# Kernel tuning notes

Measured on AMD Instinct MI355X. Metric: run time of the kernel, lower is better.

The kernel has to match this reference:

```python
import jax, jax.numpy as jnp
import numpy as np

TOTAL_WORDS = 10000
EMBED_LEN = 100
SEQ_LEN = 80
UNITS = 512
BATCH = 1024


def gru_layer(x_seq, Wx, Wh, b):
    """Keras GRU (reset_after=True), x_seq: [T, B, D] -> ys: [T, B, U]."""
    bi, br = b[0], b[1]  # input bias, recurrent bias, each [3U]
    U = Wh.shape[0]

    def step(h, x_t):
        gx = x_t @ Wx + bi            # [B, 3U]
        gh = h @ Wh + br              # [B, 3U]
        xz, xr, xh = gx[:, :U], gx[:, U:2 * U], gx[:, 2 * U:]
        hz, hr, hn = gh[:, :U], gh[:, U:2 * U], gh[:, 2 * U:]
        z = jax.nn.sigmoid(xz + hz)
        r = jax.nn.sigmoid(xr + hr)
        hh = jnp.tanh(xh + r * hn)
        h_new = z * h + (1.0 - z) * hh
        return h_new, h_new

    h0 = jnp.zeros((x_seq.shape[1], U), dtype=x_seq.dtype)
    _, ys = jax.lax.scan(step, h0, x_seq)
    return ys


def setup_inputs() -> dict:
    key = jax.random.key(0)
    ks = jax.random.split(key, 10)
    tokens = jax.random.randint(ks[0], (BATCH, SEQ_LEN), 0, TOTAL_WORDS, dtype=jnp.int32)
    s_e = 1.0 / np.sqrt(EMBED_LEN)
    s_u = 1.0 / np.sqrt(UNITS)
    emb = jax.random.normal(ks[1], (TOTAL_WORDS, EMBED_LEN), jnp.float32) * 0.05
    Wx1 = jax.random.normal(ks[2], (EMBED_LEN, 3 * UNITS), jnp.float32) * s_e
    Wh1 = jax.random.normal(ks[3], (UNITS, 3 * UNITS), jnp.float32) * s_u
    b1 = jnp.zeros((2, 3 * UNITS), jnp.float32)
    Wx2 = jax.random.normal(ks[4], (UNITS, 3 * UNITS), jnp.float32) * s_u
    Wh2 = jax.random.normal(ks[5], (UNITS, 3 * UNITS), jnp.float32) * s_u
    b2 = jnp.zeros((2, 3 * UNITS), jnp.float32)
    Wfc = jax.random.normal(ks[6], (UNITS, 1), jnp.float32) * s_u
    bfc = jnp.zeros((1,), jnp.float32)
    return {"tokens": tokens, "emb": emb, "Wx1": Wx1, "Wh1": Wh1, "b1": b1,
            "Wx2": Wx2, "Wh2": Wh2, "b2": b2, "Wfc": Wfc, "bfc": bfc}


def reference(tokens, emb, Wx1, Wh1, b1, Wx2, Wh2, b2, Wfc, bfc):
    x = emb[tokens]                       # [B, T, E]
    x = jnp.transpose(x, (1, 0, 2))       # [T, B, E] (scan over time)
    ys1 = gru_layer(x, Wx1, Wh1, b1)      # [T, B, U] return_sequences
    ys2 = gru_layer(ys1, Wx2, Wh2, b2)    # [T, B, U]
    h_last = ys2[-1]                      # [B, U] (last timestep only)
    logits = h_last @ Wfc + bfc           # [B, 1]
    return jax.nn.sigmoid(logits)
```

## Files before the change

### kernel.cpp

```cpp
#include <hip/hip_runtime.h>
#include <hip/hip_bf16.h>
#include <math.h>

typedef float f32x4 __attribute__((ext_vector_type(4)));
typedef int   ix4  __attribute__((ext_vector_type(4)));

#define MFMAI8(a,b,c) __builtin_amdgcn_mfma_i32_16x16x64_i8(a,b,c,0,0,0)

constexpr int BATCH = 1024, SEQ = 80, EMB = 100, U = 512;
constexpr int KC1 = 10;
constexpr int KC2 = 16;
constexpr float EMBMAX = 0.32f;
constexpr float INV127SQ = 1.f / 16129.f;

__device__ __forceinline__ float sigf_(float x) {
  return __builtin_amdgcn_rcpf(1.f + __expf(-x));
}
__device__ __forceinline__ float tanhf_(float x) {
  return fmaf(2.f, __builtin_amdgcn_rcpf(1.f + __expf(-2.f * x)), -1.f);
}

__global__ void k_colmax(const float* __restrict__ Wh1, const float* __restrict__ Wx1,
                         const float* __restrict__ Wh2, const float* __restrict__ Wx2,
                         float* __restrict__ scales) {
  int idx = blockIdx.x * 256 + threadIdx.x;
  if (idx >= 4 * 8 * 1536) return;
  int col = idx % 1536;
  int rest = idx / 1536;
  int kseg = rest & 7, m = rest >> 3;
  const float* W = (m == 0) ? Wh1 : (m == 1) ? Wx1 : (m == 2) ? Wh2 : Wx2;
  int Klim = (m == 1) ? EMB : 512;
  int k0 = kseg * 64, k1 = min(k0 + 64, Klim);
  float mx = 0.f;
  for (int k = k0; k < k1; ++k) mx = fmaxf(mx, fabsf(W[(size_t)k * 1536 + col]));
  if (k1 > k0) atomicMax((int*)&scales[m * 1536 + col], __float_as_int(mx));
}

__device__ __forceinline__ void pack_one(const float* __restrict__ WH,
                                         const float* __restrict__ WX,
                                         const float* __restrict__ scH,
                                         const float* __restrict__ scX,
                                         signed char* __restrict__ out,
                                         int KCH, int KCX, int KXr, int c) {
  int KC = KCH + KCX;
  int lane = c & 63;
  int rest = c >> 6;
  int g = rest % 3; rest /= 3;
  int kc = rest % KC;
  int u16 = rest / KC;
  int col = g * 512 + u16 * 16 + (lane & 15);
  int kl = (lane >> 4) * 16;
  float sH = 127.f / fmaxf(scH[col], 1e-12f);
  float sX = 127.f / fmaxf(scX[col], 1e-12f);
  ix4 v;
  signed char* vb = (signed char*)&v;
#pragma unroll
  for (int e = 0; e < 16; ++e) {
    int q = 0;
    if (kc < KCH) {
      int k = kc * 64 + kl + e;
      q = (int)rintf(WH[(size_t)k * 1536 + col] * sH);
    } else {
      int kx = (kc - KCH) * 64 + kl + e;
      if (kx < KXr) q = (int)rintf(WX[(size_t)kx * 1536 + col] * sX);
    }
    vb[e] = (signed char)q;
  }
  *(ix4*)(out + (size_t)c * 16) = v;
}

__global__ void k_prep(const float* __restrict__ Wh1, const float* __restrict__ Wx1,
                       const float* __restrict__ Wh2, const float* __restrict__ Wx2,
                       const float* __restrict__ scales,
                       signed char* __restrict__ wf1, signed char* __restrict__ wf2,
                       const float* __restrict__ emb, signed char* __restrict__ embq) {
  int b = blockIdx.x, tid = threadIdx.x;
  if (b < 240) {
    int c = b * 256 + tid;
    if (c < 61440) pack_one(Wh1, Wx1, scales, scales + 1536, wf1, 8, 2, EMB, c);
  } else if (b < 624) {
    int c = (b - 240) * 256 + tid;
    if (c < 98304) pack_one(Wh2, Wx2, scales + 3072, scales + 4608, wf2, 8, 8, U, c);
  } else {
    int idx = (b - 624) * 256 + tid;
    if (idx < 320000) {
      int r = idx >> 5, c4 = (idx & 31) * 4;
      char q[4];
#pragma unroll
      for (int j = 0; j < 4; ++j) {
        int c = c4 + j, v = 0;
        if (c < EMB) {
          float x = emb[r * EMB + c] * (127.f / EMBMAX);
          v = (int)rintf(fminf(127.f, fmaxf(-127.f, x)));
        }
        q[j] = (char)v;
      }
      *(int*)(embq + (size_t)r * 128 + c4) = *(int*)q;
    }
  }
}


__device__ __forceinline__ unsigned llc_read(const unsigned* p) {
  unsigned v;
  asm volatile("global_load_dword %0, %1, off sc0 sc1\n\ts_waitcnt vmcnt(0)"
               : "=v"(v) : "v"(p) : "memory");
  return v;
}

__device__ __forceinline__ void bar_arrive(unsigned* cnt, bool fast) {
  asm volatile("s_waitcnt vmcnt(0)" ::: "memory");
  __syncthreads();
  if (threadIdx.x == 0) {
    if (!fast) __builtin_amdgcn_fence(__ATOMIC_RELEASE, "agent");
    __hip_atomic_fetch_add(cnt, 1u, __ATOMIC_RELAXED, __HIP_MEMORY_SCOPE_AGENT);
  }
}

__device__ __forceinline__ void bar_wait(const unsigned* cnt, unsigned tgt, bool fast) {
  if (threadIdx.x == 0) {
    int spin = 0;
    while (llc_read(cnt) < tgt) {
      __builtin_amdgcn_s_sleep(1);
      if (++spin > (1 << 22)) break;
    }
    if (fast) {
      asm volatile("buffer_inv sc0\n\ts_waitcnt vmcnt(0)" ::: "memory");
    } else {
      __builtin_amdgcn_fence(__ATOMIC_ACQUIRE, "agent");
    }
  }
  __syncthreads();
}

__global__ __launch_bounds__(512, 2)
void k_gru_persist(const int* __restrict__ tokens, const signed char* __restrict__ embq,
                   const signed char* __restrict__ wf1, const signed char* __restrict__ wf2,
                   const float* __restrict__ b1, const float* __restrict__ b2,
                   const float* __restrict__ scales,
                   signed char* __restrict__ h1b0, signed char* __restrict__ h1b1,
                   signed char* __restrict__ h2b0, signed char* __restrict__ h2b1,
                   const float* __restrict__ Wfc, const float* __restrict__ bfc,
                   float* __restrict__ out, unsigned* __restrict__ bar) {
  __shared__ __attribute__((aligned(16))) signed char wt2[2 * KC2 * 3 * 1024];
  __shared__ unsigned char s_x[256];
  __shared__ int s_gl;

  const int bid = blockIdx.x, tid = threadIdx.x;

  {
    ix4* hz = (ix4*)(h1b0 + (size_t)bid * 8192);
    hz[tid] = (ix4){0, 0, 0, 0};
  }

  unsigned* xslot = bar + 1024;
  unsigned* gcnt  = bar + 1536;
  unsigned xcc = 0;
  asm volatile("s_getreg_b32 %0, hwreg(HW_REG_XCC_ID)" : "=s"(xcc));
  if (tid == 0)
    __hip_atomic_store(&xslot[bid], xcc + 1u, __ATOMIC_RELAXED, __HIP_MEMORY_SCOPE_AGENT);

  __syncthreads();
  if (tid == 0) {
    __builtin_amdgcn_fence(__ATOMIC_RELEASE, "agent");
    __hip_atomic_fetch_add(gcnt, 1u, __ATOMIC_RELAXED, __HIP_MEMORY_SCOPE_AGENT);
    int spin = 0;
    while (__hip_atomic_load(gcnt, __ATOMIC_RELAXED, __HIP_MEMORY_SCOPE_AGENT) < 256u) {
      __builtin_amdgcn_s_sleep(8);
      if (++spin > (1 << 24)) break;
    }
    __builtin_amdgcn_fence(__ATOMIC_ACQUIRE, "agent");
  }
  __syncthreads();

  if (tid < 256)
    s_x[tid] = (unsigned char)__hip_atomic_load(&xslot[tid], __ATOMIC_RELAXED,
                                                __HIP_MEMORY_SCOPE_AGENT);
  __syncthreads();
  if (tid == 0) {
    int cnts[8] = {0, 0, 0, 0, 0, 0, 0, 0};
    int r = 0;
    unsigned char mex = (unsigned char)(xcc + 1u);
    for (int b = 0; b < 256; ++b) {
      unsigned char v = s_x[b];
      if (v >= 1 && v <= 8) cnts[v - 1]++;
      if (b < bid && v == mex) r++;
    }
    int ok = 1;
    for (int j = 0; j < 8; ++j) ok &= (cnts[j] == 32);
    int gg, ll;
    if (ok) { gg = (int)xcc * 2 + (r >> 4); ll = r & 15; }
    else    { gg = bid & 15;                ll = bid >> 4; }
    s_gl = (gg << 9) | (ll << 1) | ok;
  }
  __syncthreads();
  const int g = s_gl >> 9, lb = (s_gl >> 1) & 15;
  const bool fastbar = (s_gl & 1) != 0;
  const int r0 = g * 64;
  unsigned* cnt1 = bar + g * 64;
  unsigned* cnt2 = bar + g * 64 + 32;

  {
    const ix4* s2 = (const ix4*)(wf2 + (size_t)lb * 6144 * 16);
    ix4* d2 = (ix4*)wt2;
    for (int i = tid; i < 6144; i += 512) d2[i] = s2[i];
  }

  const int wv = tid >> 6, lane = tid & 63, ln = lane & 15, quad = lane >> 4;
  const int rt = wv >> 1, uh = wv & 1;
  const int u16 = lb * 2 + uh;
  const int rw0 = r0 + rt * 16;
  const int kq = quad * 16;

  ix4 w1[30];
  {
    const ix4* s1 = (const ix4*)(wf1 + (size_t)u16 * KC1 * 3 * 1024);
#pragma unroll
    for (int f = 0; f < 30; ++f) w1[f] = s1[f * 64 + lane];
  }
  const signed char* wt2h = wt2 + uh * (KC2 * 3 * 1024) + lane * 16;

  const int u = u16 * 16 + ln;
  const float* sc_h1 = scales, *sc_x1 = scales + 1536, *sc_h2 = scales + 3072, *sc_x2 = scales + 4608;
  const float fz1h = sc_h1[u] * INV127SQ,        fz1x = sc_x1[u] * (EMBMAX * INV127SQ);
  const float fr1h = sc_h1[512 + u] * INV127SQ,  fr1x = sc_x1[512 + u] * (EMBMAX * INV127SQ);
  const float fn1h = sc_h1[1024 + u] * INV127SQ, fn1x = sc_x1[1024 + u] * (EMBMAX * INV127SQ);
  const float fz2h = sc_h2[u] * INV127SQ,        fz2x = sc_x2[u] * INV127SQ;
  const float fr2h = sc_h2[512 + u] * INV127SQ,  fr2x = sc_x2[512 + u] * INV127SQ;
  const float fn2h = sc_h2[1024 + u] * INV127SQ, fn2x = sc_x2[1024 + u] * INV127SQ;
  const float bz1 = b1[u] + b1[1536 + u],       br1 = b1[512 + u] + b1[2048 + u];
  const float bn1x = b1[1024 + u],              bn1h = b1[2560 + u];
  const float bz2 = b2[u] + b2[1536 + u],       br2 = b2[512 + u] + b2[2048 + u];
  const float bn2x = b2[1024 + u],              bn2h = b2[2560 + u];
  const size_t wb8 = (size_t)(u >> 6) * 65536 + (u & 63);

  float h1st[4] = {0.f, 0.f, 0.f, 0.f};
  float h2st[4] = {0.f, 0.f, 0.f, 0.f};

  ix4 z1x = (ix4){0,0,0,0}, r1x = (ix4){0,0,0,0}, n1x = (ix4){0,0,0,0};
  {
    int tok = tokens[(size_t)(rw0 + ln) * SEQ];
#pragma unroll
    for (int kc = 0; kc < 2; ++kc) {
      ix4 a = *(const ix4*)(embq + (size_t)tok * 128 + kc * 64 + kq);
      z1x = MFMAI8(a, w1[(8 + kc) * 3 + 0], z1x);
      r1x = MFMAI8(a, w1[(8 + kc) * 3 + 1], r1x);
      n1x = MFMAI8(a, w1[(8 + kc) * 3 + 2], n1x);
    }
  }

#pragma unroll 1
  for (int s = 0; s <= SEQ; ++s) {
    const signed char* h1r = (s & 1) ? h1b0 : h1b1;
    signed char*       h1w = (s & 1) ? h1b1 : h1b0;
    const signed char* h2r = (s & 1) ? h2b1 : h2b0;
    signed char*       h2w = (s & 1) ? h2b0 : h2b1;

    bar_wait(cnt1, 16u * (unsigned)s, fastbar);

    ix4 z1h = (ix4){0,0,0,0}, r1h = (ix4){0,0,0,0}, n1h = (ix4){0,0,0,0};
    ix4 z2x = (ix4){0,0,0,0}, r2x = (ix4){0,0,0,0}, n2x = (ix4){0,0,0,0};
#pragma unroll
    for (int kc = 0; kc < 8; ++kc) {
      ix4 a = *(const ix4*)(h1r + (size_t)kc * 65536 + (rw0 + ln) * 64 + kq);
      z1h = MFMAI8(a, w1[kc * 3 + 0], z1h);
      r1h = MFMAI8(a, w1[kc * 3 + 1], r1h);
      n1h = MFMAI8(a, w1[kc * 3 + 2], n1h);
      z2x = MFMAI8(a, *(const ix4*)(wt2h + ((8 + kc) * 3 + 0) * 1024), z2x);
      r2x = MFMAI8(a, *(const ix4*)(wt2h + ((8 + kc) * 3 + 1) * 1024), r2x);
      n2x = MFMAI8(a, *(const ix4*)(wt2h + ((8 + kc) * 3 + 2) * 1024), n2x);
    }
    if (s < SEQ) {
#pragma unroll
      for (int i = 0; i < 4; ++i) {
        int row = rw0 + quad * 4 + i;
        float z = sigf_(fmaf(fz1h, (float)z1h[i], fmaf(fz1x, (float)z1x[i], bz1)));
        float r = sigf_(fmaf(fr1h, (float)r1h[i], fmaf(fr1x, (float)r1x[i], br1)));
        float hh = tanhf_(fmaf(fn1x, (float)n1x[i], bn1x) +
                          r * fmaf(fn1h, (float)n1h[i], bn1h));
        float hn = hh + z * (h1st[i] - hh);
        h1st[i] = hn;
        h1w[wb8 + (size_t)row * 64] = (signed char)(int)rintf(hn * 127.f);
      }
    }
    bar_arrive(cnt1, fastbar);

    bar_wait(cnt2, 16u * (unsigned)s, fastbar);

    ix4 z2h = (ix4){0,0,0,0}, r2h = (ix4){0,0,0,0}, n2h = (ix4){0,0,0,0};
#pragma unroll
    for (int kc = 0; kc < 8; ++kc) {
      ix4 a = *(const ix4*)(h2r + (size_t)kc * 65536 + (rw0 + ln) * 64 + kq);
      z2h = MFMAI8(a, *(const ix4*)(wt2h + (kc * 3 + 0) * 1024), z2h);
      r2h = MFMAI8(a, *(const ix4*)(wt2h + (kc * 3 + 1) * 1024), r2h);
      n2h = MFMAI8(a, *(const ix4*)(wt2h + (kc * 3 + 2) * 1024), n2h);
    }
    if (s >= 1) {
#pragma unroll
      for (int i = 0; i < 4; ++i) {
        int row = rw0 + quad * 4 + i;
        float z = sigf_(fmaf(fz2h, (float)z2h[i], fmaf(fz2x, (float)z2x[i], bz2)));
        float r = sigf_(fmaf(fr2h, (float)r2h[i], fmaf(fr2x, (float)r2x[i], br2)));
        float hh = tanhf_(fmaf(fn2x, (float)n2x[i], bn2x) +
                          r * fmaf(fn2h, (float)n2h[i], bn2h));
        float hn = hh + z * (h2st[i] - hh);
        h2st[i] = hn;
        h2w[wb8 + (size_t)row * 64] = (signed char)(int)rintf(hn * 127.f);
      }
    }
    bar_arrive(cnt2, fastbar);

    if (s < SEQ - 1) {
      int tok = tokens[(size_t)(rw0 + ln) * SEQ + (s + 1)];
      z1x = (ix4){0,0,0,0}; r1x = (ix4){0,0,0,0}; n1x = (ix4){0,0,0,0};
#pragma unroll
      for (int kc = 0; kc < 2; ++kc) {
        ix4 a = *(const ix4*)(embq + (size_t)tok * 128 + kc * 64 + kq);
        z1x = MFMAI8(a, w1[(8 + kc) * 3 + 0], z1x);
        r1x = MFMAI8(a, w1[(8 + kc) * 3 + 1], r1x);
        n1x = MFMAI8(a, w1[(8 + kc) * 3 + 2], n1x);
      }
    }
  }

  bar_wait(cnt2, 16u * (unsigned)(SEQ + 1), fastbar);

  if (wv < 4) {
    int row = r0 + lb * 4 + wv;
    float sfc = 0.f;
#pragma unroll
    for (int j = 0; j < 8; ++j) {
      int k = j * 64 + lane;
      sfc += (float)h2b1[(size_t)j * 65536 + row * 64 + lane] * Wfc[k];
    }
#pragma unroll
    for (int off = 32; off; off >>= 1) sfc += __shfl_down(sfc, off, 64);
    if (lane == 0) out[row] = sigf_(sfc * (1.f / 127.f) + bfc[0]);
  }
}

extern "C" void kernel_launch(void* const* d_in, const int* in_sizes, int n_in,
                              void* d_out, int out_size, void* d_ws, size_t ws_size,
                              hipStream_t stream) {
  const int*   tokens = (const int*)d_in[0];
  const float* emb = (const float*)d_in[1];
  const float* Wx1 = (const float*)d_in[2];
  const float* Wh1 = (const float*)d_in[3];
  const float* b1  = (const float*)d_in[4];
  const float* Wx2 = (const float*)d_in[5];
  const float* Wh2 = (const float*)d_in[6];
  const float* b2  = (const float*)d_in[7];
  const float* Wfc = (const float*)d_in[8];
  const float* bfc = (const float*)d_in[9];
  float* out = (float*)d_out;

  signed char* wf1  = (signed char*)d_ws;
  signed char* wf2  = wf1 + 983040;
  signed char* embq = wf2 + 1572864;
  float* scales     = (float*)(embq + 1280000);
  unsigned* bar     = (unsigned*)((signed char*)scales + 24576);
  signed char* h1b0 = (signed char*)bar + 8192;
  signed char* h1b1 = h1b0 + 524288;
  signed char* h2b0 = h1b1 + 524288;
  signed char* h2b1 = h2b0 + 524288;

  hipMemsetAsync(scales, 0, 24576 + 8192, stream);

  k_colmax<<<(4 * 8 * 1536 + 255) / 256, 256, 0, stream>>>(Wh1, Wx1, Wh2, Wx2, scales);
  k_prep<<<1874, 256, 0, stream>>>(Wh1, Wx1, Wh2, Wx2, scales, wf1, wf2, emb, embq);

  void* args[] = {(void*)&tokens, (void*)&embq, (void*)&wf1, (void*)&wf2,
                  (void*)&b1, (void*)&b2, (void*)&scales,
                  (void*)&h1b0, (void*)&h1b1, (void*)&h2b0, (void*)&h2b1,
                  (void*)&Wfc, (void*)&bfc, (void*)&out, (void*)&bar};
  hipLaunchCooperativeKernel((void*)k_gru_persist, dim3(256), dim3(512), args, 0, stream);
}
```

Measured before the change: 587.2 us.

## Merge two per-step group barriers into one and unroll timestep pairs

Each timestep previously used two barriers: layer 1 finished and published h1 before layer 2 read h2. Now both h1 and h2 fragments are loaded right after a single barrier wait, all MFMAs for both layers are issued, and one arrive ends the step. This is possible because layer 2 at step s reads only h2 from step s-1. The loop is also unrolled in pairs through a macro so the ping-pong buffer pointers are fixed at compile time, and the XCC-aware group remapping is replaced by a fixed bid&15 grouping with a same-XCC check that decides whether the fast barrier is used. The cost is more live registers for the preloaded A fragments, and possibly fewer groups qualifying for the fast barrier path.

```diff
diff --git a/kernel.cpp b/kernel.cpp
--- a/kernel.cpp
+++ b/kernel.cpp
@@ -147,6 +147,9 @@
   __shared__ int s_gl;
 
   const int bid = blockIdx.x, tid = threadIdx.x;
+  const int g = bid & 15, lb = bid >> 4;
+  const int r0 = g * 64;
+  unsigned* cnt = bar + g * 64;
 
   {
     ix4* hz = (ix4*)(h1b0 + (size_t)bid * 8192);
@@ -178,27 +181,13 @@
                                                 __HIP_MEMORY_SCOPE_AGENT);
   __syncthreads();
   if (tid == 0) {
-    int cnts[8] = {0, 0, 0, 0, 0, 0, 0, 0};
-    int r = 0;
-    unsigned char mex = (unsigned char)(xcc + 1u);
-    for (int b = 0; b < 256; ++b) {
-      unsigned char v = s_x[b];
-      if (v >= 1 && v <= 8) cnts[v - 1]++;
-      if (b < bid && v == mex) r++;
-    }
-    int ok = 1;
-    for (int j = 0; j < 8; ++j) ok &= (cnts[j] == 32);
-    int gg, ll;
-    if (ok) { gg = (int)xcc * 2 + (r >> 4); ll = r & 15; }
-    else    { gg = bid & 15;                ll = bid >> 4; }
-    s_gl = (gg << 9) | (ll << 1) | ok;
-  }
-  __syncthreads();
-  const int g = s_gl >> 9, lb = (s_gl >> 1) & 15;
-  const bool fastbar = (s_gl & 1) != 0;
-  const int r0 = g * 64;
-  unsigned* cnt1 = bar + g * 64;
-  unsigned* cnt2 = bar + g * 64 + 32;
+    unsigned char x0 = s_x[g];
+    int f = (x0 != 0);
+    for (int j = 1; j < 16; ++j) f &= (s_x[g + 16 * j] == x0);
+    s_gl = f;
+  }
+  __syncthreads();
+  const bool fastbar = (s_gl != 0);
 
   {
     const ix4* s2 = (const ix4*)(wf2 + (size_t)lb * 6144 * 16);
@@ -211,6 +200,7 @@
   const int u16 = lb * 2 + uh;
   const int rw0 = r0 + rt * 16;
   const int kq = quad * 16;
+  const int aoff = (rw0 + ln) * 64 + kq;
 
   ix4 w1[30];
   {
@@ -249,81 +239,83 @@
     }
   }
 
+#define GRU_STEP(S, H1R, H1W, H2R, H2W)                                        \
+  {                                                                            \
+    bar_wait(cnt, 16u * (unsigned)(S), fastbar);                               \
+    ix4 a1[8], a2[8];                                                          \
+    _Pragma("unroll")                                                          \
+    for (int kc = 0; kc < 8; ++kc)                                             \
+      a1[kc] = *(const ix4*)((H1R) + (size_t)kc * 65536 + aoff);               \
+    _Pragma("unroll")                                                          \
+    for (int kc = 0; kc < 8; ++kc)                                             \
+      a2[kc] = *(const ix4*)((H2R) + (size_t)kc * 65536 + aoff);               \
+    ix4 z1h = (ix4){0,0,0,0}, r1h = (ix4){0,0,0,0}, n1h = (ix4){0,0,0,0};      \
+    ix4 z2x = (ix4){0,0,0,0}, r2x = (ix4){0,0,0,0}, n2x = (ix4){0,0,0,0};      \
+    ix4 z2h = (ix4){0,0,0,0}, r2h = (ix4){0,0,0,0}, n2h = (ix4){0,0,0,0};      \
+    _Pragma("unroll")                                                          \
+    for (int kc = 0; kc < 8; ++kc) {                                           \
+      z1h = MFMAI8(a1[kc], w1[kc * 3 + 0], z1h);                               \
+      r1h = MFMAI8(a1[kc], w1[kc * 3 + 1], r1h);                               \
+      n1h = MFMAI8(a1[kc], w1[kc * 3 + 2], n1h);                               \
+      z2x = MFMAI8(a1[kc], *(const ix4*)(wt2h + ((8 + kc) * 3 + 0) * 1024), z2x); \
+      r2x = MFMAI8(a1[kc], *(const ix4*)(wt2h + ((8 + kc) * 3 + 1) * 1024), r2x); \
+      n2x = MFMAI8(a1[kc], *(const ix4*)(wt2h + ((8 + kc) * 3 + 2) * 1024), n2x); \
+    }                                                                          \
+    _Pragma("unroll")                                                          \
+    for (int kc = 0; kc < 8; ++kc) {                                           \
+      z2h = MFMAI8(a2[kc], *(const ix4*)(wt2h + (kc * 3 + 0) * 1024), z2h);    \
+      r2h = MFMAI8(a2[kc], *(const ix4*)(wt2h + (kc * 3 + 1) * 1024), r2h);    \
+      n2h = MFMAI8(a2[kc], *(const ix4*)(wt2h + (kc * 3 + 2) * 1024), n2h);    \
+    }                                                                          \
+    if ((S) < SEQ) {                                                           \
+      _Pragma("unroll")                                                        \
+      for (int i = 0; i < 4; ++i) {                                            \
+        int row = rw0 + quad * 4 + i;                                          \
+        float z = sigf_(fmaf(fz1h, (float)z1h[i], fmaf(fz1x, (float)z1x[i], bz1))); \
+        float r = sigf_(fmaf(fr1h, (float)r1h[i], fmaf(fr1x, (float)r1x[i], br1))); \
+        float hh = tanhf_(fmaf(fn1x, (float)n1x[i], bn1x) +                    \
+                          r * fmaf(fn1h, (float)n1h[i], bn1h));                \
+        float hn = hh + z * (h1st[i] - hh);                                    \
+        h1st[i] = hn;                                                          \
+        (H1W)[wb8 + (size_t)row * 64] = (signed char)(int)rintf(hn * 127.f);   \
+      }                                                                        \
+    }                                                                          \
+    if ((S) >= 1) {                                                            \
+      _Pragma("unroll")                                                        \
+      for (int i = 0; i < 4; ++i) {                                            \
+        int row = rw0 + quad * 4 + i;                                          \
+        float z = sigf_(fmaf(fz2h, (float)z2h[i], fmaf(fz2x, (float)z2x[i], bz2))); \
+        float r = sigf_(fmaf(fr2h, (float)r2h[i], fmaf(fr2x, (float)r2x[i], br2))); \
+        float hh = tanhf_(fmaf(fn2x, (float)n2x[i], bn2x) +                    \
+                          r * fmaf(fn2h, (float)n2h[i], bn2h));                \
+        float hn = hh + z * (h2st[i] - hh);                                    \
+        h2st[i] = hn;                                                          \
+        (H2W)[wb8 + (size_t)row * 64] = (signed char)(int)rintf(hn * 127.f);   \
+      }                                                                        \
+    }                                                                          \
+    bar_arrive(cnt, fastbar);                                                  \
+    if ((S) < SEQ - 1) {                                                       \
+      int tok = tokens[(size_t)(rw0 + ln) * SEQ + ((S) + 1)];                  \
+      z1x = (ix4){0,0,0,0}; r1x = (ix4){0,0,0,0}; n1x = (ix4){0,0,0,0};        \
+      _Pragma("unroll")                                                        \
+      for (int kc = 0; kc < 2; ++kc) {                                         \
+        ix4 a = *(const ix4*)(embq + (size_t)tok * 128 + kc * 64 + kq);        \
+        z1x = MFMAI8(a, w1[(8 + kc) * 3 + 0], z1x);                            \
+        r1x = MFMAI8(a, w1[(8 + kc) * 3 + 1], r1x);                            \
+        n1x = MFMAI8(a, w1[(8 + kc) * 3 + 2], n1x);                            \
+      }                                                                        \
+    }                                                                          \
+  }
+
 #pragma unroll 1
-  for (int s = 0; s <= SEQ; ++s) {
-    const signed char* h1r = (s & 1) ? h1b0 : h1b1;
-    signed char*       h1w = (s & 1) ? h1b1 : h1b0;
-    const signed char* h2r = (s & 1) ? h2b1 : h2b0;
-    signed char*       h2w = (s & 1) ? h2b0 : h2b1;
-
-    bar_wait(cnt1, 16u * (unsigned)s, fastbar);
-
-    ix4 z1h = (ix4){0,0,0,0}, r1h = (ix4){0,0,0,0}, n1h = (ix4){0,0,0,0};
-    ix4 z2x = (ix4){0,0,0,0}, r2x = (ix4){0,0,0,0}, n2x = (ix4){0,0,0,0};
-#pragma unroll
-    for (int kc = 0; kc < 8; ++kc) {
-      ix4 a = *(const ix4*)(h1r + (size_t)kc * 65536 + (rw0 + ln) * 64 + kq);
-      z1h = MFMAI8(a, w1[kc * 3 + 0], z1h);
-      r1h = MFMAI8(a, w1[kc * 3 + 1], r1h);
-      n1h = MFMAI8(a, w1[kc * 3 + 2], n1h);
-      z2x = MFMAI8(a, *(const ix4*)(wt2h + ((8 + kc) * 3 + 0) * 1024), z2x);
-      r2x = MFMAI8(a, *(const ix4*)(wt2h + ((8 + kc) * 3 + 1) * 1024), r2x);
-      n2x = MFMAI8(a, *(const ix4*)(wt2h + ((8 + kc) * 3 + 2) * 1024), n2x);
-    }
-    if (s < SEQ) {
-#pragma unroll
-      for (int i = 0; i < 4; ++i) {
-        int row = rw0 + quad * 4 + i;
-        float z = sigf_(fmaf(fz1h, (float)z1h[i], fmaf(fz1x, (float)z1x[i], bz1)));
-        float r = sigf_(fmaf(fr1h, (float)r1h[i], fmaf(fr1x, (float)r1x[i], br1)));
-        float hh = tanhf_(fmaf(fn1x, (float)n1x[i], bn1x) +
-                          r * fmaf(fn1h, (float)n1h[i], bn1h));
-        float hn = hh + z * (h1st[i] - hh);
-        h1st[i] = hn;
-        h1w[wb8 + (size_t)row * 64] = (signed char)(int)rintf(hn * 127.f);
-      }
-    }
-    bar_arrive(cnt1, fastbar);
-
-    bar_wait(cnt2, 16u * (unsigned)s, fastbar);
-
-    ix4 z2h = (ix4){0,0,0,0}, r2h = (ix4){0,0,0,0}, n2h = (ix4){0,0,0,0};
-#pragma unroll
-    for (int kc = 0; kc < 8; ++kc) {
-      ix4 a = *(const ix4*)(h2r + (size_t)kc * 65536 + (rw0 + ln) * 64 + kq);
-      z2h = MFMAI8(a, *(const ix4*)(wt2h + (kc * 3 + 0) * 1024), z2h);
-      r2h = MFMAI8(a, *(const ix4*)(wt2h + (kc * 3 + 1) * 1024), r2h);
-      n2h = MFMAI8(a, *(const ix4*)(wt2h + (kc * 3 + 2) * 1024), n2h);
-    }
-    if (s >= 1) {
-#pragma unroll
-      for (int i = 0; i < 4; ++i) {
-        int row = rw0 + quad * 4 + i;
-        float z = sigf_(fmaf(fz2h, (float)z2h[i], fmaf(fz2x, (float)z2x[i], bz2)));
-        float r = sigf_(fmaf(fr2h, (float)r2h[i], fmaf(fr2x, (float)r2x[i], br2)));
-        float hh = tanhf_(fmaf(fn2x, (float)n2x[i], bn2x) +
-                          r * fmaf(fn2h, (float)n2h[i], bn2h));
-        float hn = hh + z * (h2st[i] - hh);
-        h2st[i] = hn;
-        h2w[wb8 + (size_t)row * 64] = (signed char)(int)rintf(hn * 127.f);
-      }
-    }
-    bar_arrive(cnt2, fastbar);
-
-    if (s < SEQ - 1) {
-      int tok = tokens[(size_t)(rw0 + ln) * SEQ + (s + 1)];
-      z1x = (ix4){0,0,0,0}; r1x = (ix4){0,0,0,0}; n1x = (ix4){0,0,0,0};
-#pragma unroll
-      for (int kc = 0; kc < 2; ++kc) {
-        ix4 a = *(const ix4*)(embq + (size_t)tok * 128 + kc * 64 + kq);
-        z1x = MFMAI8(a, w1[(8 + kc) * 3 + 0], z1x);
-        r1x = MFMAI8(a, w1[(8 + kc) * 3 + 1], r1x);
-        n1x = MFMAI8(a, w1[(8 + kc) * 3 + 2], n1x);
-      }
-    }
-  }
-
-  bar_wait(cnt2, 16u * (unsigned)(SEQ + 1), fastbar);
+  for (int sb = 0; sb < SEQ; sb += 2) {
+    GRU_STEP(sb,     h1b1, h1b0, h2b0, h2b1);
+    GRU_STEP(sb + 1, h1b0, h1b1, h2b1, h2b0);
+  }
+  GRU_STEP(SEQ, h1b1, h1b0, h2b0, h2b1);
+#undef GRU_STEP
+
+  bar_wait(cnt, 16u * (unsigned)(SEQ + 1), fastbar);
 
   if (wv < 4) {
     int row = r0 + lb * 4 + wv;
```

Result: slower. 851.7 us (+45.1%).
